# Performance work log

Measured on AMD Instinct MI355X. Metric: run time of the kernel, lower is better.

Reference implementation:

```python
import jax, jax.numpy as jnp
import numpy as np

UP = 16  # up_scale
EPS = 1e-5


def conv2d(x, w, b, pad):
    # x: [N,C,H,W], w: [O,I,kh,kw]
    out = jax.lax.conv_general_dilated(
        x, w, window_strides=(1, 1), padding=[(pad, pad), (pad, pad)],
        dimension_numbers=("NCHW", "OIHW", "NCHW"))
    return out + b[None, :, None, None]


def batchnorm(x, gamma, beta):
    # torch BatchNorm2d training mode: biased batch stats over (N,H,W)
    mu = jnp.mean(x, axis=(0, 2, 3), keepdims=True)
    var = jnp.var(x, axis=(0, 2, 3), keepdims=True)
    xn = (x - mu) * jax.lax.rsqrt(var + EPS)
    return xn * gamma[None, :, None, None] + beta[None, :, None, None]


def unfold3x3(x):
    # F.unfold(x, [3,3], padding=1) -> [N, C, 9, H, W] with (kh,kw) row-major order
    N, C, H, W = x.shape
    xp = jnp.pad(x, ((0, 0), (0, 0), (1, 1), (1, 1)))
    patches = [xp[:, :, i:i + H, j:j + W] for i in range(3) for j in range(3)]
    return jnp.stack(patches, axis=2)


def setup_inputs() -> dict:
    key = jax.random.key(0)
    ks = jax.random.split(key, 14)
    N, Cin, H, W = 4, 128, 64, 64
    Cout = 2
    s = 0.05
    inp = {
        "img_f": jax.random.normal(ks[0], (N, Cin, H, W), jnp.float32),
        # flowhead: conv3x3 -> BN -> ReLU -> conv3x3
        "fh_w1": jax.random.normal(ks[1], (Cout, Cin, 3, 3), jnp.float32) * s,
        "fh_b1": jax.random.normal(ks[2], (Cout,), jnp.float32) * s,
        "fh_g": jnp.ones((Cout,), jnp.float32),
        "fh_beta": jnp.zeros((Cout,), jnp.float32),
        "fh_w2": jax.random.normal(ks[3], (Cout, Cout, 3, 3), jnp.float32) * s,
        "fh_b2": jax.random.normal(ks[4], (Cout,), jnp.float32) * s,
        # mask head: conv3x3 -> BN -> ReLU -> conv1x1
        "mk_w1": jax.random.normal(ks[5], (UP * UP, Cin, 3, 3), jnp.float32) * s,
        "mk_b1": jax.random.normal(ks[6], (UP * UP,), jnp.float32) * s,
        "mk_g": jnp.ones((UP * UP,), jnp.float32),
        "mk_beta": jnp.zeros((UP * UP,), jnp.float32),
        "mk_w2": jax.random.normal(ks[7], (UP * UP * 9, UP * UP, 1, 1), jnp.float32) * s,
        "mk_b2": jax.random.normal(ks[8], (UP * UP * 9,), jnp.float32) * s,
    }
    return inp


def reference(img_f, fh_w1, fh_b1, fh_g, fh_beta, fh_w2, fh_b2,
              mk_w1, mk_b1, mk_g, mk_beta, mk_w2, mk_b2):
    # flow head
    h = conv2d(img_f, fh_w1, fh_b1, pad=1)
    h = jax.nn.relu(batchnorm(h, fh_g, fh_beta))
    flow = conv2d(h, fh_w2, fh_b2, pad=1)          # [N, C, H, W]

    # mask head
    m = conv2d(img_f, mk_w1, mk_b1, pad=1)
    m = jax.nn.relu(batchnorm(m, mk_g, mk_beta))
    mask = conv2d(m, mk_w2, mk_b2, pad=0) * 0.25   # [N, 9*UP*UP, H, W]

    N, C, H, W = flow.shape
    mask = mask.reshape(N, 1, 9, UP, UP, H, W)
    mask = jax.nn.softmax(mask, axis=2)

    up_flow = unfold3x3(8.0 * flow)                # [N, C, 9, H, W]
    up_flow = up_flow[:, :, :, None, None, :, :]   # [N, C, 9, 1, 1, H, W]
    up_flow = jnp.sum(mask * up_flow, axis=2)      # [N, C, UP, UP, H, W]
    up_flow = jnp.transpose(up_flow, (0, 1, 4, 2, 5, 3))  # [N, C, H, UP, W, UP]
    return up_flow.reshape(N, C, UP * H, UP * W)
```

## Files before the change

kernel.cpp:

```cpp
#include <hip/hip_runtime.h>
#include <hip/hip_bf16.h>

#define N_B   4
#define C_IN  128
#define HWSZ  4096
#define C_M   256

typedef __attribute__((ext_vector_type(8))) short          s16x8;
typedef __attribute__((ext_vector_type(8))) unsigned short u16x8;
typedef __attribute__((ext_vector_type(4))) unsigned short u16x4;
typedef __attribute__((ext_vector_type(4))) float          f32x4;

__device__ __forceinline__ unsigned short f2bf(float f) {
    union { float f; unsigned u; } v; v.f = f;
    unsigned r = v.u + 0x7fffu + ((v.u >> 16) & 1u);
    return (unsigned short)(r >> 16);
}
__device__ __forceinline__ float bf2f(unsigned short u) {
    union { unsigned u; float f; } v; v.u = ((unsigned)u) << 16; return v.f;
}

__global__ void __launch_bounds__(256)
prep_all(const float* __restrict__ img,
         const float* __restrict__ mk_w1, const float* __restrict__ fh_w1,
         const float* __restrict__ mk_w2,
         unsigned short* __restrict__ imgT,
         unsigned short* __restrict__ w1f, unsigned short* __restrict__ w2f)
{
    __shared__ float s[128][65];
    const int b = blockIdx.x;
    if (b < 256) {
        const int n = b >> 6, h = b & 63;
        const float* src = img + (size_t)n * C_IN * HWSZ + h * 64;
        for (int i = threadIdx.x; i < 128 * 64; i += 256) {
            int ci = i >> 6, w = i & 63;
            s[ci][w] = src[(size_t)ci * HWSZ + w];
        }
        __syncthreads();
        unsigned short* dst = imgT + ((size_t)(n * 64 + h) * 64) * 128;
        for (int i = threadIdx.x; i < 64 * 128; i += 256) {
            int w = i >> 7, ci = i & 127;
            dst[(size_t)w * 128 + ci] = f2bf(s[ci][w]);
        }
        return;
    }
    int i = (b - 256) * 256 + threadIdx.x;
    if (i < 2304 * 256) {
        int uvt = i / 36864;
        int r   = i - uvt * 36864;
        int k   = r / 4096;
        int r2  = r - k * 4096;
        int ks  = r2 >> 9;
        int lg  = (r2 >> 7) & 3;
        int ln  = (r2 >> 3) & 15;
        int j   = r2 & 7;
        w2f[i] = f2bf(0.25f * mk_w2[(size_t)(k * 256 + uvt * 16 + ln) * 256 + ks * 32 + lg * 8 + j]);
    }
    if (i < 2 * 4 * 9 * 9 * 512) {
        int z   = i / 165888;
        int r   = i - z * 165888;
        int cc  = r / 41472;
        int r2  = r - cc * 41472;
        int tap = r2 / 4608;
        int r3  = r2 - tap * 4608;
        int g   = r3 / 512;
        int r4  = r3 - g * 512;
        int lane = r4 >> 3, j = r4 & 7;
        int lg = lane >> 4, ln = lane & 15;
        int row = g * 16 + ln;
        int ci  = cc * 32 + lg * 8 + j;
        float w = 0.f;
        if (z == 0) {
            if (row < 128)      w = mk_w1[((size_t)row * C_IN + ci) * 9 + tap];
            else if (row < 130) w = fh_w1[((size_t)(row - 128) * C_IN + ci) * 9 + tap];
        } else {
            if (row < 128)      w = mk_w1[((size_t)(128 + row) * C_IN + ci) * 9 + tap];
        }
        w1f[i] = f2bf(w);
    }
}

__global__ void __launch_bounds__(512, 4)
conv1_mfma(const unsigned short* __restrict__ imgT,
           const unsigned short* __restrict__ w1f,
           const float* __restrict__ mk_b1, const float* __restrict__ fh_b1,
           unsigned short* __restrict__ m_frag, float* __restrict__ h_pre,
           float* __restrict__ ps_s, float* __restrict__ ps_s2)
{
    __shared__ unsigned short s_img[3][66][40];
    __shared__ float s_bias[144];
    __shared__ float s_ps[2][144], s_ps2[2][144];

    const int hw = blockIdx.x;
    const int xcd = hw & 7, slot = hw >> 3;
    const int lid = xcd * 64 + slot;
    const int n = lid >> 7, h = (lid >> 1) & 63, z = lid & 1;
    const int hn = n * 64 + h;

    const int tid = threadIdx.x;
    const int wv = tid >> 6, lane = tid & 63;
    const int lg = lane >> 4, ln = lane & 15;
    const int gq = wv >> 1, half = wv & 1;
    const int g0 = z ? (gq * 2) : ((int[4]){0, 3, 5, 7})[gq];
    const int gn = z ? 2 : ((int[4]){3, 2, 2, 2})[gq];

    if (tid < 144) {
        float b = 0.f;
        if (z == 0) {
            if (tid < 128)      b = mk_b1[tid];
            else if (tid < 130) b = fh_b1[tid - 128];
        } else if (tid < 128)   b = mk_b1[128 + tid];
        s_bias[tid] = b;
    }

    f32x4 acc[3][2];
#pragma unroll
    for (int g = 0; g < 3; ++g)
#pragma unroll
        for (int q = 0; q < 2; ++q) acc[g][q] = (f32x4){0.f, 0.f, 0.f, 0.f};

    for (int cc = 0; cc < 4; ++cc) {
        __syncthreads();
        for (int i = tid; i < 3 * 66 * 4; i += 512) {
            int r = i / 264;
            int rem = i - r * 264;
            int c = rem >> 2, un = rem & 3;
            int gy = h - 1 + r, gx = c - 1;
            u16x8 v = {0, 0, 0, 0, 0, 0, 0, 0};
            if ((unsigned)gy < 64u && (unsigned)gx < 64u)
                v = *(const u16x8*)&imgT[((size_t)((n * 64 + gy) * 64 + gx)) * 128 + cc * 32 + un * 8];
            *(u16x8*)&s_img[r][c][un * 8] = v;
        }
        __syncthreads();

        const unsigned short* wfp = w1f + (size_t)(z * 4 + cc) * 81 * 512 + lane * 8;
#pragma unroll
        for (int tap = 0; tap < 9; ++tap) {
            const int dy = tap / 3, dx = tap % 3;
            s16x8 bf[2];
#pragma unroll
            for (int q = 0; q < 2; ++q)
                bf[q] = *(const s16x8*)&s_img[dy][half * 32 + q * 16 + ln + dx][lg * 8];
#pragma unroll
            for (int gi = 0; gi < 3; ++gi) {
                if (gi < gn) {
                    s16x8 af = *(const s16x8*)&wfp[(size_t)(tap * 9 + g0 + gi) * 512];
#pragma unroll
                    for (int q = 0; q < 2; ++q)
                        acc[gi][q] = __builtin_amdgcn_mfma_f32_16x16x32_bf16(af, bf[q], acc[gi][q], 0, 0, 0);
                }
            }
        }
    }

#pragma unroll
    for (int gi = 0; gi < 3; ++gi) {
        if (gi >= gn) continue;
        const int g = g0 + gi;
        float v[2][4];
#pragma unroll
        for (int q = 0; q < 2; ++q)
#pragma unroll
            for (int r = 0; r < 4; ++r)
                v[q][r] = acc[gi][q][r] + s_bias[g * 16 + lg * 4 + r];
#pragma unroll
        for (int q = 0; q < 2; ++q) {
            const int px  = half * 32 + q * 16 + ln;
            const int pxg = h * 4 + half * 2 + q;
            if (z == 0 && g == 8) {
                if (lg == 0) {
#pragma unroll
                    for (int r = 0; r < 2; ++r)
                        h_pre[((size_t)(n * 2 + r)) * HWSZ + h * 64 + px] = v[q][r];
                }
            } else {
                u16x4 vv;
#pragma unroll
                for (int r = 0; r < 4; ++r) vv[r] = f2bf(v[q][r]);
                int ks  = z * 4 + (g >> 1);
                int lgp = ((g & 1) * 2 + (lg >> 1)) & 3;
                size_t off = ((((size_t)(n * 256 + pxg) * 8 + ks) * 4 + lgp) * 128) + ln * 8 + (lg & 1) * 4;
                *(u16x4*)&m_frag[off] = vv;
            }
        }
#pragma unroll
        for (int r = 0; r < 4; ++r) {
            float s  = v[0][r] + v[1][r];
            float s2 = v[0][r] * v[0][r] + v[1][r] * v[1][r];
#pragma unroll
            for (int off = 1; off < 16; off <<= 1) {
                s  += __shfl_xor(s,  off, 64);
                s2 += __shfl_xor(s2, off, 64);
            }
            if (ln == 0) {
                s_ps[half][g * 16 + lg * 4 + r]  = s;
                s_ps2[half][g * 16 + lg * 4 + r] = s2;
            }
        }
    }
    __syncthreads();
    const int nch = z ? 128 : 130;
    if (tid < nch) {
        const int idx = z * 146 + tid;
        ps_s[(size_t)idx * 256 + hn]  = s_ps[0][tid] + s_ps[1][tid];
        ps_s2[(size_t)idx * 256 + hn] = s_ps2[0][tid] + s_ps2[1][tid];
    }
}

__global__ void __launch_bounds__(64)
bn_final2(const float* __restrict__ ps_s, const float* __restrict__ ps_s2,
          const float* __restrict__ mk_g, const float* __restrict__ mk_be,
          const float* __restrict__ fh_g, const float* __restrict__ fh_be,
          float* __restrict__ ab_m, float* __restrict__ ab_h)
{
    const int b = blockIdx.x;
    const int idx = (b < 256) ? ((b >> 7) * 146 + (b & 127)) : (128 + (b - 256));
    const int t = threadIdx.x;
    float S = 0.f, S2 = 0.f;
    const float* p1 = ps_s  + (size_t)idx * 256;
    const float* p2 = ps_s2 + (size_t)idx * 256;
    for (int i = t; i < 256; i += 64) { S += p1[i]; S2 += p2[i]; }
#pragma unroll
    for (int off = 32; off > 0; off >>= 1) {
        S += __shfl_down(S, off, 64); S2 += __shfl_down(S2, off, 64);
    }
    if (t == 0) {
        const float inv = 1.0f / (float)(N_B * HWSZ);
        float mu = S * inv;
        float var = S2 * inv - mu * mu;
        float r = rsqrtf(var + 1e-5f);
        if (b < 256) {
            float a = mk_g[b] * r;
            ab_m[2 * b] = a; ab_m[2 * b + 1] = mk_be[b] - mu * a;
        } else {
            int c = b - 256;
            float a = fh_g[c] * r;
            ab_h[2 * c] = a; ab_h[2 * c + 1] = fh_be[c] - mu * a;
        }
    }
}

__global__ void __launch_bounds__(256)
bnrelu_flow(unsigned short* __restrict__ m_frag, const float* __restrict__ ab,
            const float* __restrict__ hpre, const float* __restrict__ ab_h,
            const float* __restrict__ w2, const float* __restrict__ b2,
            float* __restrict__ flow8)
{
    __shared__ float s_ab[512];
    const int t = threadIdx.x;
    if (blockIdx.x < 2048) {
        s_ab[t] = ab[t]; s_ab[256 + t] = ab[256 + t];
        __syncthreads();
        const unsigned u = blockIdx.x * 256 + t;
        const int lg = (u >> 4) & 3, ks = (u >> 7) & 7;
        const int cb = ks * 32 + lg * 8;
        u16x8 v = *(const u16x8*)&m_frag[(size_t)u * 8];
        u16x8 o;
#pragma unroll
        for (int j = 0; j < 8; ++j) {
            float a = s_ab[2 * (cb + j)], b = s_ab[2 * (cb + j) + 1];
            o[j] = f2bf(fmaxf(a * bf2f(v[j]) + b, 0.f));
        }
        *(u16x8*)&m_frag[(size_t)u * 8] = o;
        return;
    }
    int idx = (blockIdx.x - 2048) * 256 + t;
    int w = idx & 63, h = (idx >> 6) & 63, co = (idx >> 12) & 1, n = idx >> 13;
    float acc = b2[co];
#pragma unroll
    for (int ci = 0; ci < 2; ++ci) {
        float a = ab_h[2 * ci], b = ab_h[2 * ci + 1];
        const float* p = hpre + (size_t)(n * 2 + ci) * HWSZ;
        const float* wp = &w2[(co * 2 + ci) * 9];
#pragma unroll
        for (int dy = 0; dy < 3; ++dy)
#pragma unroll
            for (int dx = 0; dx < 3; ++dx) {
                int gy = h + dy - 1, gx = w + dx - 1;
                float v = 0.f;
                if ((unsigned)gy < 64u && (unsigned)gx < 64u)
                    v = fmaxf(a * p[gy * 64 + gx] + b, 0.f);
                acc += wp[dy * 3 + dx] * v;
            }
    }
    flow8[idx] = acc * 8.0f;
}

__global__ void __launch_bounds__(1024, 4)
mask_combine_mfma(const unsigned short* __restrict__ m_frag,
                  const unsigned short* __restrict__ w2f,
                  const float* __restrict__ mk_b2,
                  const float* __restrict__ flow8,
                  float* __restrict__ out)
{
    __shared__ unsigned short s_w[36864];
    __shared__ float s_o[2][8192];
    __shared__ float s_fl[2][18][66];
    __shared__ float s_bias[9][16];

    const int id = blockIdx.x;
    const int uvt = id >> 4, r4 = id & 15;
    const int hg = r4 & 3, n = r4 >> 2;

    const int tid = threadIdx.x;
    const int wv = tid >> 6, lane = tid & 63;
    const int lg = lane >> 4, ln = lane & 15;
    const int row_l = wv >> 2, qq = wv & 3;
    const int w = qq * 16 + ln;

    {
        const u16x8* wsrc = (const u16x8*)(w2f + (size_t)uvt * 36864);
        u16x8* wdst = (u16x8*)s_w;
        for (int i = tid; i < 4608; i += 1024) wdst[i] = wsrc[i];
    }
    for (int i = tid; i < 2 * 18 * 66; i += 1024) {
        int c = i / 1188, rem = i - c * 1188, r = rem / 66, col = rem - r * 66;
        int gy = hg * 16 - 1 + r, gx = col - 1;
        float v = 0.f;
        if ((unsigned)gy < 64u && (unsigned)gx < 64u)
            v = flow8[((size_t)(n * 2 + c)) * HWSZ + gy * 64 + gx];
        s_fl[c][r][col] = v;
    }
    if (tid < 144) s_bias[tid >> 4][tid & 15] = 0.25f * mk_b2[(tid >> 4) * 256 + uvt * 16 + (tid & 15)];
    __syncthreads();

    const unsigned short* wk0 = s_w + lg * 128 + ln * 8;
    const unsigned short* mb0 = m_frag + (size_t)(n * 256 + (hg * 16 + row_l) * 4 + qq) * 4096
                              + lg * 128 + ln * 8;

    s16x8 bq[4];
#pragma unroll
    for (int d = 0; d < 4; ++d) bq[d] = *(const s16x8*)&mb0[d * 512];

    for (int pass = 0; pass < 4; ++pass) {
        const unsigned short* mb = mb0 + (size_t)pass * 65536;

        f32x4 acc[9];
#pragma unroll
        for (int k = 0; k < 9; ++k) acc[k] = (f32x4){0.f, 0.f, 0.f, 0.f};

#pragma unroll
        for (int ks = 0; ks < 8; ++ks) {
            const int d = ks & 3;
            const unsigned short* wk = wk0 + ks * 512;
#pragma unroll
            for (int k = 0; k < 9; ++k) {
                s16x8 af = *(const s16x8*)&wk[k * 4096];
                acc[k] = __builtin_amdgcn_mfma_f32_16x16x32_bf16(af, bq[d], acc[k], 0, 0, 0);
            }
            if (ks < 4) bq[d] = *(const s16x8*)&mb[(ks + 4) * 512];
        }
        if (pass < 3) {
#pragma unroll
            for (int d = 0; d < 4; ++d)
                bq[d] = *(const s16x8*)&mb[65536 + d * 512];
        }

        float* so = s_o[pass & 1];

#pragma unroll
        for (int r = 0; r < 4; ++r) {
            const int vv = lg * 4 + r;
            float p[9], sum = 0.f;
#pragma unroll
            for (int k = 0; k < 9; ++k) {
                p[k] = __expf(acc[k][r] + s_bias[k][vv]);
                sum += p[k];
            }
            float inv = 1.0f / sum;
            float a0 = 0.f, a1 = 0.f;
#pragma unroll
            for (int k = 0; k < 9; ++k) {
                const int dy = k / 3, dx = k % 3;
                a0 += p[k] * s_fl[0][pass * 4 + row_l + dy][w + dx];
                a1 += p[k] * s_fl[1][pass * 4 + row_l + dy][w + dx];
            }
            so[(0 * 4 + row_l) * 1024 + w * 16 + vv] = a0 * inv;
            so[(1 * 4 + row_l) * 1024 + w * 16 + vv] = a1 * inv;
        }
        __syncthreads();

        for (int i = tid; i < 2048; i += 1024) {
            const int idx = i * 4;
            const int row = idx >> 10;
            const int col = idx & 1023;
            const int c = row >> 2, rl = row & 3;
            f32x4 v = *(const f32x4*)&so[idx];
            *(f32x4*)(out + ((size_t)(n * 2 + c) * 1024 +
                             (hg * 16 + pass * 4 + rl) * 16 + uvt) * 1024 + col) = v;
        }
    }
}

extern "C" void kernel_launch(void* const* d_in, const int* in_sizes, int n_in,
                              void* d_out, int out_size, void* d_ws, size_t ws_size,
                              hipStream_t stream) {
    const float* img   = (const float*)d_in[0];
    const float* fh_w1 = (const float*)d_in[1];
    const float* fh_b1 = (const float*)d_in[2];
    const float* fh_g  = (const float*)d_in[3];
    const float* fh_be = (const float*)d_in[4];
    const float* fh_w2 = (const float*)d_in[5];
    const float* fh_b2 = (const float*)d_in[6];
    const float* mk_w1 = (const float*)d_in[7];
    const float* mk_b1 = (const float*)d_in[8];
    const float* mk_g  = (const float*)d_in[9];
    const float* mk_be = (const float*)d_in[10];
    const float* mk_w2 = (const float*)d_in[11];
    const float* mk_b2 = (const float*)d_in[12];
    float* out = (float*)d_out;

    char* p = (char*)d_ws;
    unsigned short* w2f    = (unsigned short*)p;  p += (size_t)1179648;
    unsigned short* w1f    = (unsigned short*)p;  p += (size_t)663552;
    unsigned short* imgT   = (unsigned short*)p;  p += (size_t)4194304;
    unsigned short* m_frag = (unsigned short*)p;  p += (size_t)8388608;
    float* h_pre  = (float*)p;  p += (size_t)131072;
    float* flow8  = (float*)p;  p += (size_t)131072;
    float* ps_s   = (float*)p;  p += (size_t)280576;
    float* ps_s2  = (float*)p;  p += (size_t)280576;
    float* ab_m   = (float*)p;  p += 2048;
    float* ab_h   = (float*)p;  p += 64;

    prep_all<<<2560, 256, 0, stream>>>(img, mk_w1, fh_w1, mk_w2, imgT, w1f, w2f);
    conv1_mfma<<<512, 512, 0, stream>>>(imgT, w1f, mk_b1, fh_b1, m_frag, h_pre, ps_s, ps_s2);
    bn_final2<<<258, 64, 0, stream>>>(ps_s, ps_s2, mk_g, mk_be, fh_g, fh_be, ab_m, ab_h);
    bnrelu_flow<<<2176, 256, 0, stream>>>(m_frag, ab_m, h_pre, ab_h, fh_w2, fh_b2, flow8);
    mask_combine_mfma<<<256, 1024, 0, stream>>>(m_frag, w2f, mk_b2, flow8, out);
}
```

Measured before the change: 77.40 us.

## Switch mask conv to 32x32x16 MFMA with paired softmax taps and two passes

Replaces the 16x16x32 bf16 MFMA tiles (9 per k-step) in the mask/combine kernel with 32x32x16 tiles, where each tile covers two of the nine softmax taps and one tile is padded with zeros. The weight prep is rewritten to emit this new A-fragment layout. Each wave now covers 32 pixels, and the work is done in 2 passes of 8 rows instead of 4 passes of 4. Flow neighbours are hoisted into registers and the softmax-weighted sum is fused into one loop. The goal is fewer MFMA issues and fewer LDS weight reads per unit of work, at the cost of about 11% wasted MFMA work on the padding tile, a larger single output buffer that needs an extra barrier, and more accumulator registers.

Result: no change. 78.25 us (+1.1%).

```diff
diff --git a/kernel.cpp b/kernel.cpp
--- a/kernel.cpp
+++ b/kernel.cpp
@@ -6,10 +6,11 @@
 #define HWSZ  4096
 #define C_M   256
 
-typedef __attribute__((ext_vector_type(8))) short          s16x8;
-typedef __attribute__((ext_vector_type(8))) unsigned short u16x8;
-typedef __attribute__((ext_vector_type(4))) unsigned short u16x4;
-typedef __attribute__((ext_vector_type(4))) float          f32x4;
+typedef __attribute__((ext_vector_type(8)))  short          s16x8;
+typedef __attribute__((ext_vector_type(8)))  unsigned short u16x8;
+typedef __attribute__((ext_vector_type(4)))  unsigned short u16x4;
+typedef __attribute__((ext_vector_type(4)))  float          f32x4;
+typedef __attribute__((ext_vector_type(16))) float          f32x16;
 
 __device__ __forceinline__ unsigned short f2bf(float f) {
     union { float f; unsigned u; } v; v.f = f;
@@ -25,7 +26,7 @@
          const float* __restrict__ mk_w1, const float* __restrict__ fh_w1,
          const float* __restrict__ mk_w2,
          unsigned short* __restrict__ imgT,
-         unsigned short* __restrict__ w1f, unsigned short* __restrict__ w2f)
+         unsigned short* __restrict__ w1f, unsigned short* __restrict__ w2a)
 {
     __shared__ float s[128][65];
     const int b = blockIdx.x;
@@ -45,16 +46,20 @@
         return;
     }
     int i = (b - 256) * 256 + threadIdx.x;
-    if (i < 2304 * 256) {
-        int uvt = i / 36864;
-        int r   = i - uvt * 36864;
-        int k   = r / 4096;
-        int r2  = r - k * 4096;
-        int ks  = r2 >> 9;
-        int lg  = (r2 >> 7) & 3;
-        int ln  = (r2 >> 3) & 15;
-        int j   = r2 & 7;
-        w2f[i] = f2bf(0.25f * mk_w2[(size_t)(k * 256 + uvt * 16 + ln) * 256 + ks * 32 + lg * 8 + j]);
+    if (i < 16 * 40960) {
+        int uvt = i / 40960;
+        int r   = i - uvt * 40960;
+        int t   = r / 8192;
+        int r2  = r - t * 8192;
+        int ks16 = r2 >> 9;
+        int lane = (r2 >> 3) & 63;
+        int j    = r2 & 7;
+        int k9 = t * 2 + ((lane >> 4) & 1);
+        int uv = lane & 15;
+        int c  = ks16 * 16 + (lane >> 5) * 8 + j;
+        w2a[i] = (k9 < 9)
+            ? f2bf(0.25f * mk_w2[((size_t)(k9 * 256 + uvt * 16 + uv)) * 256 + c])
+            : (unsigned short)0;
     }
     if (i < 2 * 4 * 9 * 9 * 512) {
         int z   = i / 165888;
@@ -288,13 +293,13 @@
 
 __global__ void __launch_bounds__(1024, 4)
 mask_combine_mfma(const unsigned short* __restrict__ m_frag,
-                  const unsigned short* __restrict__ w2f,
+                  const unsigned short* __restrict__ w2a,
                   const float* __restrict__ mk_b2,
                   const float* __restrict__ flow8,
                   float* __restrict__ out)
 {
-    __shared__ unsigned short s_w[36864];
-    __shared__ float s_o[2][8192];
+    __shared__ unsigned short s_w[40960];
+    __shared__ float s_o[16384];
     __shared__ float s_fl[2][18][66];
     __shared__ float s_bias[9][16];
 
@@ -304,91 +309,95 @@
 
     const int tid = threadIdx.x;
     const int wv = tid >> 6, lane = tid & 63;
-    const int lg = lane >> 4, ln = lane & 15;
-    const int row_l = wv >> 2, qq = wv & 3;
-    const int w = qq * 16 + ln;
+    const int row_l = wv >> 1, qhalf = wv & 1;
+    const int col = lane & 31, hi = lane >> 5;
+    const int px = qhalf * 32 + col;
 
     {
-        const u16x8* wsrc = (const u16x8*)(w2f + (size_t)uvt * 36864);
+        const u16x8* wsrc = (const u16x8*)(w2a + (size_t)uvt * 40960);
         u16x8* wdst = (u16x8*)s_w;
-        for (int i = tid; i < 4608; i += 1024) wdst[i] = wsrc[i];
+        for (int i = tid; i < 5120; i += 1024) wdst[i] = wsrc[i];
     }
     for (int i = tid; i < 2 * 18 * 66; i += 1024) {
-        int c = i / 1188, rem = i - c * 1188, r = rem / 66, col = rem - r * 66;
-        int gy = hg * 16 - 1 + r, gx = col - 1;
+        int c = i / 1188, rem = i - c * 1188, r = rem / 66, cl = rem - r * 66;
+        int gy = hg * 16 - 1 + r, gx = cl - 1;
         float v = 0.f;
         if ((unsigned)gy < 64u && (unsigned)gx < 64u)
             v = flow8[((size_t)(n * 2 + c)) * HWSZ + gy * 64 + gx];
-        s_fl[c][r][col] = v;
+        s_fl[c][r][cl] = v;
     }
     if (tid < 144) s_bias[tid >> 4][tid & 15] = 0.25f * mk_b2[(tid >> 4) * 256 + uvt * 16 + (tid & 15)];
     __syncthreads();
 
-    const unsigned short* wk0 = s_w + lg * 128 + ln * 8;
-    const unsigned short* mb0 = m_frag + (size_t)(n * 256 + (hg * 16 + row_l) * 4 + qq) * 4096
-                              + lg * 128 + ln * 8;
+    const int pxg0 = (hg * 16 + row_l) * 4 + qhalf * 2 + ((lane >> 4) & 1);
+    const unsigned short* mb0 = m_frag + ((size_t)(n * 256 + pxg0)) * 4096
+                              + hi * 128 + (lane & 15) * 8;
 
     s16x8 bq[4];
 #pragma unroll
-    for (int d = 0; d < 4; ++d) bq[d] = *(const s16x8*)&mb0[d * 512];
-
-    for (int pass = 0; pass < 4; ++pass) {
-        const unsigned short* mb = mb0 + (size_t)pass * 65536;
-
-        f32x4 acc[9];
-#pragma unroll
-        for (int k = 0; k < 9; ++k) acc[k] = (f32x4){0.f, 0.f, 0.f, 0.f};
-
-#pragma unroll
-        for (int ks = 0; ks < 8; ++ks) {
-            const int d = ks & 3;
-            const unsigned short* wk = wk0 + ks * 512;
+    for (int d = 0; d < 4; ++d) bq[d] = *(const s16x8*)&mb0[d * 256];
+
+    for (int pass = 0; pass < 2; ++pass) {
+        const unsigned short* mb = mb0 + (size_t)pass * 131072;
+
+        f32x16 acc[5];
+#pragma unroll
+        for (int t = 0; t < 5; ++t)
+#pragma unroll
+            for (int e = 0; e < 16; ++e) acc[t][e] = 0.f;
+
+#pragma unroll
+        for (int ks16 = 0; ks16 < 16; ++ks16) {
+            const int d = ks16 & 3;
+#pragma unroll
+            for (int t = 0; t < 5; ++t) {
+                s16x8 af = *(const s16x8*)&s_w[(t * 16 + ks16) * 512 + lane * 8];
+                acc[t] = __builtin_amdgcn_mfma_f32_32x32x16_bf16(af, bq[d], acc[t], 0, 0, 0);
+            }
+            if (ks16 < 12) bq[d] = *(const s16x8*)&mb[(ks16 + 4) * 256];
+        }
+        if (pass < 1) {
+#pragma unroll
+            for (int d = 0; d < 4; ++d)
+                bq[d] = *(const s16x8*)&mb[131072 + d * 256];
+        }
+
+        float fl0[9], fl1[9];
+#pragma unroll
+        for (int k = 0; k < 9; ++k) {
+            const int dy = k / 3, dx = k % 3;
+            fl0[k] = s_fl[0][pass * 8 + row_l + dy][px + dx];
+            fl1[k] = s_fl[1][pass * 8 + row_l + dy][px + dx];
+        }
+
+#pragma unroll
+        for (int i = 0; i < 8; ++i) {
+            const int uvl = hi * 4 + (i & 3) + 8 * (i >> 2);
+            float sum = 0.f, a0 = 0.f, a1 = 0.f;
 #pragma unroll
             for (int k = 0; k < 9; ++k) {
-                s16x8 af = *(const s16x8*)&wk[k * 4096];
-                acc[k] = __builtin_amdgcn_mfma_f32_16x16x32_bf16(af, bq[d], acc[k], 0, 0, 0);
-            }
-            if (ks < 4) bq[d] = *(const s16x8*)&mb[(ks + 4) * 512];
-        }
-        if (pass < 3) {
-#pragma unroll
-            for (int d = 0; d < 4; ++d)
-                bq[d] = *(const s16x8*)&mb[65536 + d * 512];
-        }
-
-        float* so = s_o[pass & 1];
-
-#pragma unroll
-        for (int r = 0; r < 4; ++r) {
-            const int vv = lg * 4 + r;
-            float p[9], sum = 0.f;
-#pragma unroll
-            for (int k = 0; k < 9; ++k) {
-                p[k] = __expf(acc[k][r] + s_bias[k][vv]);
-                sum += p[k];
+                const int reg = (i & 3) + 4 * (i >> 2) + 8 * (k & 1);
+                float e = __expf(acc[k >> 1][reg] + s_bias[k][uvl]);
+                sum += e;
+                a0 += e * fl0[k];
+                a1 += e * fl1[k];
             }
             float inv = 1.0f / sum;
-            float a0 = 0.f, a1 = 0.f;
-#pragma unroll
-            for (int k = 0; k < 9; ++k) {
-                const int dy = k / 3, dx = k % 3;
-                a0 += p[k] * s_fl[0][pass * 4 + row_l + dy][w + dx];
-                a1 += p[k] * s_fl[1][pass * 4 + row_l + dy][w + dx];
-            }
-            so[(0 * 4 + row_l) * 1024 + w * 16 + vv] = a0 * inv;
-            so[(1 * 4 + row_l) * 1024 + w * 16 + vv] = a1 * inv;
-        }
-        __syncthreads();
-
-        for (int i = tid; i < 2048; i += 1024) {
+            s_o[(0 * 8 + row_l) * 1024 + px * 16 + uvl] = a0 * inv;
+            s_o[(1 * 8 + row_l) * 1024 + px * 16 + uvl] = a1 * inv;
+        }
+        __syncthreads();
+
+        for (int i = tid; i < 4096; i += 1024) {
             const int idx = i * 4;
             const int row = idx >> 10;
-            const int col = idx & 1023;
-            const int c = row >> 2, rl = row & 3;
-            f32x4 v = *(const f32x4*)&so[idx];
+            const int cl  = idx & 1023;
+            const int c = row >> 3, rl = row & 7;
+            f32x4 v = *(const f32x4*)&s_o[idx];
             *(f32x4*)(out + ((size_t)(n * 2 + c) * 1024 +
-                             (hg * 16 + pass * 4 + rl) * 16 + uvt) * 1024 + col) = v;
-        }
+                             (hg * 16 + pass * 8 + rl) * 16 + uvt) * 1024 + cl) = v;
+        }
+        __syncthreads();
     }
 }
 
@@ -411,7 +420,7 @@
     float* out = (float*)d_out;
 
     char* p = (char*)d_ws;
-    unsigned short* w2f    = (unsigned short*)p;  p += (size_t)1179648;
+    unsigned short* w2a    = (unsigned short*)p;  p += (size_t)1310720;
     unsigned short* w1f    = (unsigned short*)p;  p += (size_t)663552;
     unsigned short* imgT   = (unsigned short*)p;  p += (size_t)4194304;
     unsigned short* m_frag = (unsigned short*)p;  p += (size_t)8388608;
@@ -422,9 +431,9 @@
     float* ab_m   = (float*)p;  p += 2048;
     float* ab_h   = (float*)p;  p += 64;
 
-    prep_all<<<2560, 256, 0, stream>>>(img, mk_w1, fh_w1, mk_w2, imgT, w1f, w2f);
+    prep_all<<<2848, 256, 0, stream>>>(img, mk_w1, fh_w1, mk_w2, imgT, w1f, w2a);
     conv1_mfma<<<512, 512, 0, stream>>>(imgT, w1f, mk_b1, fh_b1, m_frag, h_pre, ps_s, ps_s2);
     bn_final2<<<258, 64, 0, stream>>>(ps_s, ps_s2, mk_g, mk_be, fh_g, fh_be, ab_m, ab_h);
     bnrelu_flow<<<2176, 256, 0, stream>>>(m_frag, ab_m, h_pre, ab_h, fh_w2, fh_b2, flow8);
-    mask_combine_mfma<<<256, 1024, 0, stream>>>(m_frag, w2f, mk_b2, flow8, out);
-}
+    mask_combine_mfma<<<256, 1024, 0, stream>>>(m_frag, w2a, mk_b2, flow8, out);
+}
```

## Fuse image transpose into conv1 and BN-ReLU into mask combine loads

Applied to the files above, without the earlier changes.

Removes the separate image NHWC bf16 transpose pass: conv1 now reads the fp32 NCHW image directly, converts it, and writes it transposed into shared memory. It also removes the in-place BN+ReLU pass over m_frag and applies the affine and ReLU on the fly as mask_combine loads its B fragments, with the prefetch depth cut from 4 to 2. This saves two full-size global round trips and a launch. In exchange, conv1's global reads are scalar and strided per channel, mask_combine gets extra ALU work inside its MFMA loop, and the shallower prefetch may expose more load latency.

New measurement: 89.32 us. 15.4% more time.

```diff
diff --git a/kernel.cpp b/kernel.cpp
--- a/kernel.cpp
+++ b/kernel.cpp
@@ -21,30 +21,11 @@
 }
 
 __global__ void __launch_bounds__(256)
-prep_all(const float* __restrict__ img,
-         const float* __restrict__ mk_w1, const float* __restrict__ fh_w1,
-         const float* __restrict__ mk_w2,
-         unsigned short* __restrict__ imgT,
-         unsigned short* __restrict__ w1f, unsigned short* __restrict__ w2f)
+prep_weights(const float* __restrict__ mk_w1, const float* __restrict__ fh_w1,
+             const float* __restrict__ mk_w2,
+             unsigned short* __restrict__ w1f, unsigned short* __restrict__ w2f)
 {
-    __shared__ float s[128][65];
-    const int b = blockIdx.x;
-    if (b < 256) {
-        const int n = b >> 6, h = b & 63;
-        const float* src = img + (size_t)n * C_IN * HWSZ + h * 64;
-        for (int i = threadIdx.x; i < 128 * 64; i += 256) {
-            int ci = i >> 6, w = i & 63;
-            s[ci][w] = src[(size_t)ci * HWSZ + w];
-        }
-        __syncthreads();
-        unsigned short* dst = imgT + ((size_t)(n * 64 + h) * 64) * 128;
-        for (int i = threadIdx.x; i < 64 * 128; i += 256) {
-            int w = i >> 7, ci = i & 127;
-            dst[(size_t)w * 128 + ci] = f2bf(s[ci][w]);
-        }
-        return;
-    }
-    int i = (b - 256) * 256 + threadIdx.x;
+    int i = blockIdx.x * 256 + threadIdx.x;
     if (i < 2304 * 256) {
         int uvt = i / 36864;
         int r   = i - uvt * 36864;
@@ -81,7 +62,7 @@
 }
 
 __global__ void __launch_bounds__(512, 4)
-conv1_mfma(const unsigned short* __restrict__ imgT,
+conv1_mfma(const float* __restrict__ img,
            const unsigned short* __restrict__ w1f,
            const float* __restrict__ mk_b1, const float* __restrict__ fh_b1,
            unsigned short* __restrict__ m_frag, float* __restrict__ h_pre,
@@ -121,15 +102,16 @@
 
     for (int cc = 0; cc < 4; ++cc) {
         __syncthreads();
-        for (int i = tid; i < 3 * 66 * 4; i += 512) {
-            int r = i / 264;
-            int rem = i - r * 264;
-            int c = rem >> 2, un = rem & 3;
+        for (int i = tid; i < 32 * 3 * 66; i += 512) {
+            int ci  = i / 198;
+            int rem = i - ci * 198;
+            int r   = rem / 66;
+            int c   = rem - r * 66;
             int gy = h - 1 + r, gx = c - 1;
-            u16x8 v = {0, 0, 0, 0, 0, 0, 0, 0};
+            float v = 0.f;
             if ((unsigned)gy < 64u && (unsigned)gx < 64u)
-                v = *(const u16x8*)&imgT[((size_t)((n * 64 + gy) * 64 + gx)) * 128 + cc * 32 + un * 8];
-            *(u16x8*)&s_img[r][c][un * 8] = v;
+                v = img[(((size_t)(n * C_IN + cc * 32 + ci)) * 64 + gy) * 64 + gx];
+            s_img[r][c][ci] = f2bf(v);
         }
         __syncthreads();
 
@@ -241,30 +223,11 @@
 }
 
 __global__ void __launch_bounds__(256)
-bnrelu_flow(unsigned short* __restrict__ m_frag, const float* __restrict__ ab,
-            const float* __restrict__ hpre, const float* __restrict__ ab_h,
-            const float* __restrict__ w2, const float* __restrict__ b2,
-            float* __restrict__ flow8)
+flow_conv2(const float* __restrict__ hpre, const float* __restrict__ ab_h,
+           const float* __restrict__ w2, const float* __restrict__ b2,
+           float* __restrict__ flow8)
 {
-    __shared__ float s_ab[512];
-    const int t = threadIdx.x;
-    if (blockIdx.x < 2048) {
-        s_ab[t] = ab[t]; s_ab[256 + t] = ab[256 + t];
-        __syncthreads();
-        const unsigned u = blockIdx.x * 256 + t;
-        const int lg = (u >> 4) & 3, ks = (u >> 7) & 7;
-        const int cb = ks * 32 + lg * 8;
-        u16x8 v = *(const u16x8*)&m_frag[(size_t)u * 8];
-        u16x8 o;
-#pragma unroll
-        for (int j = 0; j < 8; ++j) {
-            float a = s_ab[2 * (cb + j)], b = s_ab[2 * (cb + j) + 1];
-            o[j] = f2bf(fmaxf(a * bf2f(v[j]) + b, 0.f));
-        }
-        *(u16x8*)&m_frag[(size_t)u * 8] = o;
-        return;
-    }
-    int idx = (blockIdx.x - 2048) * 256 + t;
+    int idx = blockIdx.x * 256 + threadIdx.x;
     int w = idx & 63, h = (idx >> 6) & 63, co = (idx >> 12) & 1, n = idx >> 13;
     float acc = b2[co];
 #pragma unroll
@@ -289,6 +252,7 @@
 __global__ void __launch_bounds__(1024, 4)
 mask_combine_mfma(const unsigned short* __restrict__ m_frag,
                   const unsigned short* __restrict__ w2f,
+                  const float* __restrict__ ab_m,
                   const float* __restrict__ mk_b2,
                   const float* __restrict__ flow8,
                   float* __restrict__ out)
@@ -297,6 +261,7 @@
     __shared__ float s_o[2][8192];
     __shared__ float s_fl[2][18][66];
     __shared__ float s_bias[9][16];
+    __shared__ float s_ab[512];
 
     const int id = blockIdx.x;
     const int uvt = id >> 4, r4 = id & 15;
@@ -322,15 +287,30 @@
         s_fl[c][r][col] = v;
     }
     if (tid < 144) s_bias[tid >> 4][tid & 15] = 0.25f * mk_b2[(tid >> 4) * 256 + uvt * 16 + (tid & 15)];
+    if (tid < 512) s_ab[tid] = ab_m[tid];
     __syncthreads();
 
     const unsigned short* wk0 = s_w + lg * 128 + ln * 8;
     const unsigned short* mb0 = m_frag + (size_t)(n * 256 + (hg * 16 + row_l) * 4 + qq) * 4096
                               + lg * 128 + ln * 8;
-
-    s16x8 bq[4];
-#pragma unroll
-    for (int d = 0; d < 4; ++d) bq[d] = *(const s16x8*)&mb0[d * 512];
+    const int cb0 = lg * 8;
+
+    auto ldbn = [&](const unsigned short* p, int ks) -> s16x8 {
+        u16x8 v = *(const u16x8*)p;
+        u16x8 o;
+        const int cb = ks * 32 + cb0;
+#pragma unroll
+        for (int j = 0; j < 8; ++j) {
+            float a = s_ab[2 * (cb + j)], b = s_ab[2 * (cb + j) + 1];
+            o[j] = f2bf(fmaxf(a * bf2f(v[j]) + b, 0.f));
+        }
+        union { u16x8 u; s16x8 s; } cvt; cvt.u = o;
+        return cvt.s;
+    };
+
+    s16x8 bq[2];
+    bq[0] = ldbn(&mb0[0], 0);
+    bq[1] = ldbn(&mb0[512], 1);
 
     for (int pass = 0; pass < 4; ++pass) {
         const unsigned short* mb = mb0 + (size_t)pass * 65536;
@@ -341,19 +321,18 @@
 
 #pragma unroll
         for (int ks = 0; ks < 8; ++ks) {
-            const int d = ks & 3;
+            const int d = ks & 1;
             const unsigned short* wk = wk0 + ks * 512;
 #pragma unroll
             for (int k = 0; k < 9; ++k) {
                 s16x8 af = *(const s16x8*)&wk[k * 4096];
                 acc[k] = __builtin_amdgcn_mfma_f32_16x16x32_bf16(af, bq[d], acc[k], 0, 0, 0);
             }
-            if (ks < 4) bq[d] = *(const s16x8*)&mb[(ks + 4) * 512];
+            if (ks < 6) bq[d] = ldbn(&mb[(ks + 2) * 512], ks + 2);
         }
         if (pass < 3) {
-#pragma unroll
-            for (int d = 0; d < 4; ++d)
-                bq[d] = *(const s16x8*)&mb[65536 + d * 512];
+            bq[0] = ldbn(&mb[65536 + 0], 0);
+            bq[1] = ldbn(&mb[65536 + 512], 1);
         }
 
         float* so = s_o[pass & 1];
@@ -413,7 +392,6 @@
     char* p = (char*)d_ws;
     unsigned short* w2f    = (unsigned short*)p;  p += (size_t)1179648;
     unsigned short* w1f    = (unsigned short*)p;  p += (size_t)663552;
-    unsigned short* imgT   = (unsigned short*)p;  p += (size_t)4194304;
     unsigned short* m_frag = (unsigned short*)p;  p += (size_t)8388608;
     float* h_pre  = (float*)p;  p += (size_t)131072;
     float* flow8  = (float*)p;  p += (size_t)131072;
@@ -422,9 +400,9 @@
     float* ab_m   = (float*)p;  p += 2048;
     float* ab_h   = (float*)p;  p += 64;
 
-    prep_all<<<2560, 256, 0, stream>>>(img, mk_w1, fh_w1, mk_w2, imgT, w1f, w2f);
-    conv1_mfma<<<512, 512, 0, stream>>>(imgT, w1f, mk_b1, fh_b1, m_frag, h_pre, ps_s, ps_s2);
+    prep_weights<<<2304, 256, 0, stream>>>(mk_w1, fh_w1, mk_w2, w1f, w2f);
+    conv1_mfma<<<512, 512, 0, stream>>>(img, w1f, mk_b1, fh_b1, m_frag, h_pre, ps_s, ps_s2);
     bn_final2<<<258, 64, 0, stream>>>(ps_s, ps_s2, mk_g, mk_be, fh_g, fh_be, ab_m, ab_h);
-    bnrelu_flow<<<2176, 256, 0, stream>>>(m_frag, ab_m, h_pre, ab_h, fh_w2, fh_b2, flow8);
-    mask_combine_mfma<<<256, 1024, 0, stream>>>(m_frag, w2f, mk_b2, flow8, out);
-}
+    flow_conv2<<<128, 256, 0, stream>>>(h_pre, ab_h, fh_w2, fh_b2, flow8);
+    mask_combine_mfma<<<256, 1024, 0, stream>>>(m_frag, w2f, ab_m, mk_b2, flow8, out);
+}
```
